# Optimization experiments

Measured on AMD Instinct MI355X. Metric: run time of the kernel, lower is better.

The kernel has to match this reference:

```python
import jax, jax.numpy as jnp
import numpy as np

N, P, C = 100000, 64, 128
DIST_TH = 0.1


def setup_inputs() -> dict:
    key = jax.random.key(0)
    ks = jax.random.split(key, 12)
    xyz = jax.random.uniform(ks[0], (N, 3), jnp.float32) * 10.0  # room coords in [0,10)^3
    feature = jax.random.normal(ks[1], (N, C), jnp.float32)
    center = jax.random.uniform(ks[2], (P, 3), jnp.float32) * 10.0
    normal = jax.random.normal(ks[3], (P, 3), jnp.float32)
    normal = normal / jnp.linalg.norm(normal, axis=1, keepdims=True)
    pmin = center - 1.5  # axis-aligned extent used on axes 0,1
    pmax = center + 1.5
    inp = {
        'feature': feature, 'xyz': xyz,
        'plane_center': center, 'plane_normal': normal,
        'plane_min': pmin, 'plane_max': pmax,
        'W1': jax.random.normal(ks[4], (C, 2 * C), jnp.float32) * (1.0 / np.sqrt(C)),
        's1': jnp.ones((2 * C,), jnp.float32), 'b1': jnp.zeros((2 * C,), jnp.float32),
        'W2': jax.random.normal(ks[5], (2 * C, C), jnp.float32) * (1.0 / np.sqrt(2 * C)),
        's2': jnp.ones((C,), jnp.float32), 'b2': jnp.zeros((C,), jnp.float32),
        'W3': jax.random.normal(ks[6], (C, 1), jnp.float32) * (1.0 / np.sqrt(C)),
        'b3': jnp.zeros((1,), jnp.float32),
        'Wa': jax.random.normal(ks[7], (C, C), jnp.float32) * (1.0 / np.sqrt(C)),
        'Wm': jax.random.normal(ks[8], (C, C), jnp.float32) * (1.0 / np.sqrt(C)),
        'bm': jnp.zeros((C,), jnp.float32),
    }
    return inp


def reference(feature, xyz, plane_center, plane_normal, plane_min, plane_max,
              W1, s1, b1, W2, s2, b2, W3, b3, Wa, Wm, bm):
    # pointwise MLP (shared across planes): fc1 (conv+BN+ReLU), fc2 (conv+BN+ReLU)
    h = jax.nn.relu((feature @ W1) * s1 + b1)          # [N, 2C]
    h2 = jax.nn.relu((h @ W2) * s2 + b2)               # [N, C] == plane_feature
    logit = (h2 @ W3 + b3)[:, 0]                        # [N] fc3 logits (plane_result)

    # per-plane point membership masks (dense [N, P])
    proj = xyz @ plane_normal.T                         # [N, P]
    offs = jnp.sum(plane_center * plane_normal, axis=1) # [P]
    dist_mask = jnp.abs(proj - offs[None, :]) < DIST_TH
    rng = ((xyz[:, None, 0] >= plane_min[None, :, 0]) & (xyz[:, None, 0] < plane_max[None, :, 0]) &
           (xyz[:, None, 1] >= plane_min[None, :, 1]) & (xyz[:, None, 1] < plane_max[None, :, 1]))
    mask = dist_mask & rng                              # [N, P]

    on_sel = jax.nn.sigmoid(logit) > 0.5                # [N]
    on_mask = (mask & on_sel[:, None]).astype(feature.dtype)
    off_mask = (mask & ~on_sel[:, None]).astype(feature.dtype)

    # attention pooling: masked softmax over points, per plane, per channel
    a = h2 @ Wa                                         # [N, C] att activations
    e = jnp.exp(a - jnp.max(a, axis=0, keepdims=True))  # stable exp, [N, C]
    eh = e * h2

    def att_pool(m):                                    # m: [N, P] float
        num = jnp.einsum('np,nc->pc', m, eh)
        den = jnp.einsum('np,nc->pc', m, e)
        agg = num / (den + 1e-9)                        # masked-softmax weighted sum
        return jax.nn.relu(agg @ Wm + bm)               # att_pooling.mlp (conv+ReLU)

    ori = jnp.concatenate([plane_center, plane_normal, plane_min, plane_max], axis=1)  # [P, 12]
    on_feat = jnp.concatenate([att_pool(on_mask), ori], axis=1)    # [P, C+12]
    off_feat = jnp.concatenate([att_pool(off_mask), ori], axis=1)  # [P, C+12]
    return logit, on_feat, off_feat
```

## Files before the change

kernel.cpp:

```cpp
#include <hip/hip_runtime.h>

#define NPTS 100000
#define P 64
#define C 128

typedef __bf16 bf16_t;
typedef __bf16 bf16x8 __attribute__((ext_vector_type(8)));
typedef float floatx4 __attribute__((ext_vector_type(4)));


__global__ __launch_bounds__(256) void prep_kernel(
    const float* __restrict__ W1, const float* __restrict__ s1,
    const float* __restrict__ W2, const float* __restrict__ s2,
    const float* __restrict__ Wa,
    bf16_t* __restrict__ W1t, bf16_t* __restrict__ W2t, bf16_t* __restrict__ Wat,
    float* __restrict__ acc)
{
  int i0 = blockIdx.x * blockDim.x + threadIdx.x;
  int stride = gridDim.x * blockDim.x;
  for (int i = i0; i < 256 * 128; i += stride) {
    int n = i >> 7, k = i & 127;
    W1t[i] = (bf16_t)(W1[k * 256 + n] * s1[n]);
  }
  for (int i = i0; i < 128 * 256; i += stride) {
    int n = i >> 8, k = i & 255;
    W2t[i] = (bf16_t)(W2[k * 128 + n] * s2[n]);
  }
  for (int i = i0; i < 128 * 128; i += stride) {
    int n = i >> 7, k = i & 127;
    Wat[i] = (bf16_t)(Wa[k * 128 + n]);
  }
  for (int i = i0; i < P * 512; i += stride) acc[i] = 0.f;
}

__global__ __launch_bounds__(256) void main_kernel(
    const float* __restrict__ feature, const float* __restrict__ xyz,
    const float* __restrict__ b1, const float* __restrict__ b2,
    const float* __restrict__ W3, const float* __restrict__ b3,
    const float* __restrict__ ctr, const float* __restrict__ nrm,
    const float* __restrict__ pmn, const float* __restrict__ pmx,
    const bf16_t* __restrict__ W1t, const bf16_t* __restrict__ W2t,
    const bf16_t* __restrict__ Wat,
    float* __restrict__ acc, float* __restrict__ out_logit)
{
  __shared__ __align__(16) char smem[52736];
  bf16_t* A1   = (bf16_t*)smem;
  bf16_t* Hs   = (bf16_t*)(smem + 17408);
  bf16_t* aB   = (bf16_t*)(smem + 17408);
  float*  w3S  = (float*)(smem + 51200);
  float*  xyzS = (float*)(smem + 51712);
  float*  lgS  = (float*)(smem + 52480);

  const int tid  = threadIdx.x;
  const int wave = tid >> 6, lane = tid & 63;
  const int quad = lane >> 4, l16 = lane & 15;
  const int m0 = blockIdx.x * 64;

  if (tid < 128) w3S[tid] = W3[tid];
  if (tid < 192) {
    int gi = m0 * 3 + tid;
    xyzS[tid] = (gi < NPTS * 3) ? xyz[gi] : 0.f;
  }

  for (int i = tid; i < 64 * 32; i += 256) {
    int r = i >> 5, c4 = i & 31;
    float4 v = make_float4(0.f, 0.f, 0.f, 0.f);
    if (m0 + r < NPTS) v = *(const float4*)(feature + (size_t)(m0 + r) * C + c4 * 4);
    bf16_t* dst = A1 + r * 136 + c4 * 4;
    dst[0] = (bf16_t)v.x; dst[1] = (bf16_t)v.y; dst[2] = (bf16_t)v.z; dst[3] = (bf16_t)v.w;
  }
  __syncthreads();

  const floatx4 zero4 = {0.f, 0.f, 0.f, 0.f};

  {
    floatx4 acc1[4][4];
#pragma unroll
    for (int mt = 0; mt < 4; ++mt)
#pragma unroll
      for (int nt = 0; nt < 4; ++nt) acc1[mt][nt] = zero4;
#pragma unroll
    for (int kt = 0; kt < 4; ++kt) {
      bf16x8 af[4], bfr[4];
#pragma unroll
      for (int mt = 0; mt < 4; ++mt)
        af[mt] = *(const bf16x8*)(A1 + (mt * 16 + l16) * 136 + kt * 32 + quad * 8);
#pragma unroll
      for (int nt = 0; nt < 4; ++nt)
        bfr[nt] = *(const bf16x8*)(W1t + (wave * 64 + nt * 16 + l16) * 128 + kt * 32 + quad * 8);
#pragma unroll
      for (int mt = 0; mt < 4; ++mt)
#pragma unroll
        for (int nt = 0; nt < 4; ++nt)
          acc1[mt][nt] = __builtin_amdgcn_mfma_f32_16x16x32_bf16(af[mt], bfr[nt], acc1[mt][nt], 0, 0, 0);
    }
#pragma unroll
    for (int nt = 0; nt < 4; ++nt) {
      int col = wave * 64 + nt * 16 + l16;
      float bias = b1[col];
#pragma unroll
      for (int mt = 0; mt < 4; ++mt)
#pragma unroll
        for (int r = 0; r < 4; ++r) {
          float hv = fmaxf(acc1[mt][nt][r] + bias, 0.f);
          Hs[(mt * 16 + quad * 4 + r) * 264 + col] = (bf16_t)hv;
        }
    }
  }
  __syncthreads();

  {
    floatx4 acc2[4][2];
#pragma unroll
    for (int mt = 0; mt < 4; ++mt) { acc2[mt][0] = zero4; acc2[mt][1] = zero4; }
#pragma unroll
    for (int kt = 0; kt < 8; ++kt) {
      bf16x8 af[4], bfr[2];
#pragma unroll
      for (int mt = 0; mt < 4; ++mt)
        af[mt] = *(const bf16x8*)(Hs + (mt * 16 + l16) * 264 + kt * 32 + quad * 8);
#pragma unroll
      for (int nt = 0; nt < 2; ++nt)
        bfr[nt] = *(const bf16x8*)(W2t + (wave * 32 + nt * 16 + l16) * 256 + kt * 32 + quad * 8);
#pragma unroll
      for (int mt = 0; mt < 4; ++mt)
#pragma unroll
        for (int nt = 0; nt < 2; ++nt)
          acc2[mt][nt] = __builtin_amdgcn_mfma_f32_16x16x32_bf16(af[mt], bfr[nt], acc2[mt][nt], 0, 0, 0);
    }
#pragma unroll
    for (int nt = 0; nt < 2; ++nt) {
      int col = wave * 32 + nt * 16 + l16;
      float bias = b2[col];
#pragma unroll
      for (int mt = 0; mt < 4; ++mt)
#pragma unroll
        for (int r = 0; r < 4; ++r) {
          float hv = fmaxf(acc2[mt][nt][r] + bias, 0.f);
          A1[(mt * 16 + quad * 4 + r) * 136 + col] = (bf16_t)hv;
        }
    }
  }
  __syncthreads();

  {
    floatx4 acca[4][2];
#pragma unroll
    for (int mt = 0; mt < 4; ++mt) { acca[mt][0] = zero4; acca[mt][1] = zero4; }
#pragma unroll
    for (int kt = 0; kt < 4; ++kt) {
      bf16x8 af[4], bfr[2];
#pragma unroll
      for (int mt = 0; mt < 4; ++mt)
        af[mt] = *(const bf16x8*)(A1 + (mt * 16 + l16) * 136 + kt * 32 + quad * 8);
#pragma unroll
      for (int nt = 0; nt < 2; ++nt)
        bfr[nt] = *(const bf16x8*)(Wat + (wave * 32 + nt * 16 + l16) * 128 + kt * 32 + quad * 8);
#pragma unroll
      for (int mt = 0; mt < 4; ++mt)
#pragma unroll
        for (int nt = 0; nt < 2; ++nt)
          acca[mt][nt] = __builtin_amdgcn_mfma_f32_16x16x32_bf16(af[mt], bfr[nt], acca[mt][nt], 0, 0, 0);
    }
#pragma unroll
    for (int nt = 0; nt < 2; ++nt) {
      int col = wave * 32 + nt * 16 + l16;
#pragma unroll
      for (int mt = 0; mt < 4; ++mt)
#pragma unroll
        for (int r = 0; r < 4; ++r)
          aB[(mt * 16 + quad * 4 + r) * 136 + col] = (bf16_t)acca[mt][nt][r];
    }
  }
  __syncthreads();

  {
    const int m = tid >> 2, g = tid & 3, c0g = g * 32;
    const int mg = m0 + m;
    float lsum = 0.f;
#pragma unroll 8
    for (int c = 0; c < 32; ++c)
      lsum += (float)A1[m * 136 + c0g + c] * w3S[c0g + c];
    lsum += __shfl_xor(lsum, 1);
    lsum += __shfl_xor(lsum, 2);
    if (g == 0) {
      float lg = lsum + b3[0];
      lgS[m] = lg;
      if (mg < NPTS) out_logit[mg] = lg;
    }
  }
  __syncthreads();

  {
    const float nx = nrm[lane * 3], ny = nrm[lane * 3 + 1], nz = nrm[lane * 3 + 2];
    const float offsP = ctr[lane * 3] * nx + ctr[lane * 3 + 1] * ny + ctr[lane * 3 + 2] * nz;
    const float mnx = pmn[lane * 3], mny = pmn[lane * 3 + 1];
    const float mxx = pmx[lane * 3], mxy = pmx[lane * 3 + 1];

    for (int s = 0; s < 16; ++s) {
      const int pt = wave * 16 + s;
      const bool valid = (m0 + pt) < NPTS;
      const float x = xyzS[pt * 3], y = xyzS[pt * 3 + 1], z = xyzS[pt * 3 + 2];
      const float proj = x * nx + y * ny + z * nz;
      const bool hit = valid && (fabsf(proj - offsP) < 0.1f) &&
                       (x >= mnx) && (x < mxx) && (y >= mny) && (y < mxy);
      unsigned long long mball = __ballot(hit);
      if (!mball) continue;

      const int sel = (lgS[pt] > 0.f) ? 0 : 1;
      const unsigned ap = ((const unsigned*)(aB + pt * 136))[lane];
      const unsigned hp = ((const unsigned*)(A1 + pt * 136))[lane];
      const float a0 = __uint_as_float(ap << 16);
      const float a1 = __uint_as_float(ap & 0xffff0000u);
      const float h0 = __uint_as_float(hp << 16);
      const float h1 = __uint_as_float(hp & 0xffff0000u);
      const float e0 = __expf(a0), e1 = __expf(a1);
      const float eh0 = e0 * h0, eh1 = e1 * h1;

      while (mball) {
        const int pl = __builtin_ctzll(mball);
        mball &= mball - 1;
        float* ab = acc + (size_t)pl * 512 + sel * 256;
        atomicAdd(ab + 2 * lane,           eh0);
        atomicAdd(ab + 2 * lane + 1,       eh1);
        atomicAdd(ab + 128 + 2 * lane,     e0);
        atomicAdd(ab + 128 + 2 * lane + 1, e1);
      }
    }
  }
}

__global__ __launch_bounds__(128) void finalize_kernel(
    const float* __restrict__ acc,
    const float* __restrict__ Wm, const float* __restrict__ bm,
    const float* __restrict__ ctr, const float* __restrict__ nrm,
    const float* __restrict__ pmn, const float* __restrict__ pmx,
    float* __restrict__ out)
{
  int sel = blockIdx.x >> 6, p = blockIdx.x & 63;
  int j = threadIdx.x;
  const float* ab = acc + (size_t)p * 512 + sel * 256;
  float num = ab[j], den = ab[128 + j];
  __shared__ float aggS[128];
  aggS[j] = num / (den + 1e-9f);
  __syncthreads();
  float s = bm[j];
#pragma unroll 4
  for (int c = 0; c < C; ++c) s += aggS[c] * Wm[c * C + j];
  s = fmaxf(s, 0.f);
  float* dst = out + NPTS + sel * (P * 140) + p * 140;
  dst[j] = s;
  if (j < 12) {
    float v;
    if (j < 3)      v = ctr[p * 3 + j];
    else if (j < 6) v = nrm[p * 3 + j - 3];
    else if (j < 9) v = pmn[p * 3 + j - 6];
    else            v = pmx[p * 3 + j - 9];
    dst[C + j] = v;
  }
}

extern "C" void kernel_launch(void* const* d_in, const int* in_sizes, int n_in,
                              void* d_out, int out_size, void* d_ws, size_t ws_size,
                              hipStream_t stream)
{
  const float* feature = (const float*)d_in[0];
  const float* xyz     = (const float*)d_in[1];
  const float* ctr     = (const float*)d_in[2];
  const float* nrm     = (const float*)d_in[3];
  const float* pmn     = (const float*)d_in[4];
  const float* pmx     = (const float*)d_in[5];
  const float* W1      = (const float*)d_in[6];
  const float* s1      = (const float*)d_in[7];
  const float* b1      = (const float*)d_in[8];
  const float* W2      = (const float*)d_in[9];
  const float* s2      = (const float*)d_in[10];
  const float* b2      = (const float*)d_in[11];
  const float* W3      = (const float*)d_in[12];
  const float* b3      = (const float*)d_in[13];
  const float* Wa      = (const float*)d_in[14];
  const float* Wm      = (const float*)d_in[15];
  const float* bm      = (const float*)d_in[16];
  float* out = (float*)d_out;

  char* ws = (char*)d_ws;
  bf16_t* W1t = (bf16_t*)(ws);
  bf16_t* W2t = (bf16_t*)(ws + 65536);
  bf16_t* Wat = (bf16_t*)(ws + 131072);
  float*  acc = (float*)(ws + 163840);

  prep_kernel<<<64, 256, 0, stream>>>(W1, s1, W2, s2, Wa, W1t, W2t, Wat, acc);
  main_kernel<<<(NPTS + 63) / 64, 256, 0, stream>>>(
      feature, xyz, b1, b2, W3, b3, ctr, nrm, pmn, pmx, W1t, W2t, Wat, acc, out);
  finalize_kernel<<<128, 128, 0, stream>>>(acc, Wm, bm, ctr, nrm, pmn, pmx, out);
}
```

Before: 220.7 us.

## Replace per-plane global atomics with hit lists and a separate pooling pass

Instead of atomically accumulating exp-weighted features into global per-plane accumulators for every hit, the main kernel now writes each hit point's activation and feature record once, then appends a record index per hit plane into per-plane lists. A new pool2 kernel walks each plane's list in 16 chunks, reduces in registers and shared memory, and writes partial sums that finalize adds up. This targets contention from float atomics on a small accumulator array. In exchange it adds a kernel launch, extra global traffic, and fixed list/record capacities that silently drop hits if exceeded.

Measured after the change: 353.8 us. 60.3% more time.

```diff
diff --git a/kernel.cpp b/kernel.cpp
--- a/kernel.cpp
+++ b/kernel.cpp
@@ -3,6 +3,8 @@
 #define NPTS 100000
 #define P 64
 #define C 128
+#define LIST_CAP 4096
+#define REC_CAP  65536
 
 typedef __bf16 bf16_t;
 typedef __bf16 bf16x8 __attribute__((ext_vector_type(8)));
@@ -14,7 +16,7 @@
     const float* __restrict__ W2, const float* __restrict__ s2,
     const float* __restrict__ Wa,
     bf16_t* __restrict__ W1t, bf16_t* __restrict__ W2t, bf16_t* __restrict__ Wat,
-    float* __restrict__ acc)
+    unsigned* __restrict__ cnt)
 {
   int i0 = blockIdx.x * blockDim.x + threadIdx.x;
   int stride = gridDim.x * blockDim.x;
@@ -30,7 +32,7 @@
     int n = i >> 7, k = i & 127;
     Wat[i] = (bf16_t)(Wa[k * 128 + n]);
   }
-  for (int i = i0; i < P * 512; i += stride) acc[i] = 0.f;
+  if (i0 < 128) cnt[i0] = 0;
 }
 
 __global__ __launch_bounds__(256) void main_kernel(
@@ -41,7 +43,8 @@
     const float* __restrict__ pmn, const float* __restrict__ pmx,
     const bf16_t* __restrict__ W1t, const bf16_t* __restrict__ W2t,
     const bf16_t* __restrict__ Wat,
-    float* __restrict__ acc, float* __restrict__ out_logit)
+    unsigned* __restrict__ cnt, unsigned* __restrict__ list,
+    bf16_t* __restrict__ rec, float* __restrict__ out_logit)
 {
   __shared__ __align__(16) char smem[52736];
   bf16_t* A1   = (bf16_t*)smem;
@@ -207,31 +210,77 @@
       unsigned long long mball = __ballot(hit);
       if (!mball) continue;
 
+      unsigned ridx = 0;
+      if (lane == 0) ridx = atomicAdd(&cnt[64], 1u);
+      ridx = (unsigned)__shfl((int)ridx, 0);
+
       const int sel = (lgS[pt] > 0.f) ? 0 : 1;
       const unsigned ap = ((const unsigned*)(aB + pt * 136))[lane];
       const unsigned hp = ((const unsigned*)(A1 + pt * 136))[lane];
-      const float a0 = __uint_as_float(ap << 16);
-      const float a1 = __uint_as_float(ap & 0xffff0000u);
-      const float h0 = __uint_as_float(hp << 16);
-      const float h1 = __uint_as_float(hp & 0xffff0000u);
-      const float e0 = __expf(a0), e1 = __expf(a1);
-      const float eh0 = e0 * h0, eh1 = e1 * h1;
-
-      while (mball) {
-        const int pl = __builtin_ctzll(mball);
-        mball &= mball - 1;
-        float* ab = acc + (size_t)pl * 512 + sel * 256;
-        atomicAdd(ab + 2 * lane,           eh0);
-        atomicAdd(ab + 2 * lane + 1,       eh1);
-        atomicAdd(ab + 128 + 2 * lane,     e0);
-        atomicAdd(ab + 128 + 2 * lane + 1, e1);
+      if (ridx < REC_CAP) {
+        unsigned* dst = (unsigned*)(rec + (size_t)ridx * 256);
+        dst[lane]      = ap;
+        dst[64 + lane] = hp;
+        if (hit) {
+          unsigned idx = atomicAdd(&cnt[lane], 1u);
+          if (idx < LIST_CAP)
+            list[lane * LIST_CAP + idx] = (ridx << 1) | (unsigned)sel;
+        }
       }
     }
   }
 }
 
+__global__ __launch_bounds__(256) void pool2_kernel(
+    const unsigned* __restrict__ cnt, const unsigned* __restrict__ list,
+    const bf16_t* __restrict__ rec, float* __restrict__ partial)
+{
+  const int plane = blockIdx.x >> 4;
+  const int chunk = blockIdx.x & 15;
+  const int tid = threadIdx.x, wave = tid >> 6, lane = tid & 63;
+
+  __shared__ float accS[4][128];
+  for (int i = tid; i < 512; i += 256) ((float*)accS)[i] = 0.f;
+  __syncthreads();
+
+  unsigned n = cnt[plane];
+  if (n > LIST_CAP) n = LIST_CAP;
+  const unsigned* lp = list + plane * LIST_CAP;
+
+  float nOn0 = 0, nOn1 = 0, dOn0 = 0, dOn1 = 0;
+  float nOf0 = 0, nOf1 = 0, dOf0 = 0, dOf1 = 0;
+
+  for (unsigned e = (unsigned)(chunk * 4 + wave); e < n; e += 64) {
+    const unsigned ent = lp[e];
+    const unsigned pt = ent >> 1;
+    const unsigned* r32 = (const unsigned*)(rec + (size_t)pt * 256);
+    const unsigned ap = r32[lane];
+    const unsigned hp = r32[64 + lane];
+    const float a0 = __uint_as_float(ap << 16);
+    const float a1 = __uint_as_float(ap & 0xffff0000u);
+    const float h0 = __uint_as_float(hp << 16);
+    const float h1 = __uint_as_float(hp & 0xffff0000u);
+    const float e0 = __expf(a0), e1 = __expf(a1);
+    if (!(ent & 1)) { nOn0 += e0 * h0; nOn1 += e1 * h1; dOn0 += e0; dOn1 += e1; }
+    else            { nOf0 += e0 * h0; nOf1 += e1 * h1; dOf0 += e0; dOf1 += e1; }
+  }
+
+  atomicAdd(&accS[0][lane * 2],     nOn0);
+  atomicAdd(&accS[0][lane * 2 + 1], nOn1);
+  atomicAdd(&accS[1][lane * 2],     dOn0);
+  atomicAdd(&accS[1][lane * 2 + 1], dOn1);
+  atomicAdd(&accS[2][lane * 2],     nOf0);
+  atomicAdd(&accS[2][lane * 2 + 1], nOf1);
+  atomicAdd(&accS[3][lane * 2],     dOf0);
+  atomicAdd(&accS[3][lane * 2 + 1], dOf1);
+  __syncthreads();
+
+  float* dst = partial + (size_t)blockIdx.x * 512;
+  for (int i = tid; i < 512; i += 256) dst[i] = ((float*)accS)[i];
+}
+
 __global__ __launch_bounds__(128) void finalize_kernel(
-    const float* __restrict__ acc,
+    const float* __restrict__ partial,
     const float* __restrict__ Wm, const float* __restrict__ bm,
     const float* __restrict__ ctr, const float* __restrict__ nrm,
     const float* __restrict__ pmn, const float* __restrict__ pmx,
@@ -239,8 +288,13 @@
 {
   int sel = blockIdx.x >> 6, p = blockIdx.x & 63;
   int j = threadIdx.x;
-  const float* ab = acc + (size_t)p * 512 + sel * 256;
-  float num = ab[j], den = ab[128 + j];
+  float num = 0.f, den = 0.f;
+  const float* bp = partial + (size_t)p * 16 * 512 + sel * 2 * 128;
+#pragma unroll
+  for (int k = 0; k < 16; ++k) {
+    num += bp[k * 512 + j];
+    den += bp[k * 512 + 128 + j];
+  }
   __shared__ float aggS[128];
   aggS[j] = num / (den + 1e-9f);
   __syncthreads();
@@ -284,13 +338,18 @@
   float* out = (float*)d_out;
 
   char* ws = (char*)d_ws;
-  bf16_t* W1t = (bf16_t*)(ws);
-  bf16_t* W2t = (bf16_t*)(ws + 65536);
-  bf16_t* Wat = (bf16_t*)(ws + 131072);
-  float*  acc = (float*)(ws + 163840);
-
-  prep_kernel<<<64, 256, 0, stream>>>(W1, s1, W2, s2, Wa, W1t, W2t, Wat, acc);
+  bf16_t*   W1t  = (bf16_t*)(ws);
+  bf16_t*   W2t  = (bf16_t*)(ws + 65536);
+  bf16_t*   Wat  = (bf16_t*)(ws + 131072);
+  unsigned* cnt  = (unsigned*)(ws + 163840);
+  unsigned* list = (unsigned*)(ws + 164352);
+  bf16_t*   rec  = (bf16_t*)(ws + 1212928);
+  float* partial = (float*)(ws + 1212928 + (size_t)REC_CAP * 512);
+
+  prep_kernel<<<64, 256, 0, stream>>>(W1, s1, W2, s2, Wa, W1t, W2t, Wat, cnt);
   main_kernel<<<(NPTS + 63) / 64, 256, 0, stream>>>(
-      feature, xyz, b1, b2, W3, b3, ctr, nrm, pmn, pmx, W1t, W2t, Wat, acc, out);
-  finalize_kernel<<<128, 128, 0, stream>>>(acc, Wm, bm, ctr, nrm, pmn, pmx, out);
-}
+      feature, xyz, b1, b2, W3, b3, ctr, nrm, pmn, pmx,
+      W1t, W2t, Wat, cnt, list, rec, out);
+  pool2_kernel<<<64 * 16, 256, 0, stream>>>(cnt, list, rec, partial);
+  finalize_kernel<<<128, 128, 0, stream>>>(partial, Wm, bm, ctr, nrm, pmn, pmx, out);
+}
```
